# Kernel optimization log

Measured on AMD Instinct MI355X. Metric: run time of the kernel, lower is better.

Reference implementation:

```python
import jax, jax.numpy as jnp
import numpy as np

N = 8192      # number of patches (nodes)
DIN = 384     # input feature dim
DH = 512      # hidden dim
K = 6         # topk neighbors
NC = 2        # n_classes


def setup_inputs() -> dict:
    key = jax.random.key(0)
    ks = jax.random.split(key, 20)
    def w(k, shape):
        fan_in = shape[0]
        return jax.random.normal(k, shape, dtype=jnp.float32) * (1.0 / np.sqrt(fan_in))
    return {
        "x_s":   jax.random.normal(ks[0], (N, DIN), dtype=jnp.float32),
        "fc1_w": w(ks[1], (DIN, DH)), "fc1_b": jnp.zeros((DH,), jnp.float32),
        "wh_w":  w(ks[2], (DH, DH)),  "wh_b":  jnp.zeros((DH,), jnp.float32),
        "wt_w":  w(ks[3], (DH, DH)),  "wt_b":  jnp.zeros((DH,), jnp.float32),
        "l1_w":  w(ks[4], (DH, DH)),  "l1_b":  jnp.zeros((DH,), jnp.float32),
        "l2_w":  w(ks[5], (DH, DH)),  "l2_b":  jnp.zeros((DH,), jnp.float32),
        "att1_w": w(ks[6], (DH, DH // 2)), "att1_b": jnp.zeros((DH // 2,), jnp.float32),
        "att2_w": w(ks[7], (DH // 2, 1)),  "att2_b": jnp.zeros((1,), jnp.float32),
        "ln_g":  jnp.ones((DH,), jnp.float32), "ln_b": jnp.zeros((DH,), jnp.float32),
        "fc_w":  w(ks[8], (DH, NC)), "fc_b": jnp.zeros((NC,), jnp.float32),
    }


def reference(x_s, fc1_w, fc1_b, wh_w, wh_b, wt_w, wt_b,
              l1_w, l1_b, l2_w, l2_b, att1_w, att1_b, att2_w, att2_b,
              ln_g, ln_b, fc_w, fc_b):
    lrelu = jax.nn.leaky_relu  # negative_slope=0.01, torch default
    # _fc1 + mean-centering mix (batch dim of 1 dropped; mean is over nodes)
    x = lrelu(x_s @ fc1_w + fc1_b)                       # [N, DH]
    x = (x + x.mean(axis=0, keepdims=True)) * 0.5
    e_h = x @ wh_w + wh_b                                # [N, DH]
    e_t = x @ wt_w + wt_b                                # [N, DH]
    scale = DH ** -0.5
    attn_logit = (e_h * scale) @ e_t.T                   # [N, N] dense scores
    topk_w, topk_i = jax.lax.top_k(attn_logit, K)        # [N, K]
    Nb_h = e_t[topk_i]                                   # gather neighbors [N, K, DH]
    p = jax.nn.softmax(topk_w, axis=1)[..., None]        # [N, K, 1]
    eh_r = p * Nb_h + (1.0 - p) * e_h[:, None, :]        # outer-product form == broadcast
    gate = jnp.tanh(e_h[:, None, :] + eh_r)              # [N, K, DH]
    ka = jnp.einsum('nkd,nkd->nk', Nb_h, gate)           # [N, K]
    ka_p = jax.nn.softmax(ka, axis=1)
    e_Nh = jnp.einsum('nk,nkd->nd', ka_p, Nb_h)          # [N, DH]
    # bi-interaction aggregation (dropout = identity in eval)
    emb = lrelu((e_h + e_Nh) @ l1_w + l1_b) + lrelu((e_h * e_Nh) @ l2_w + l2_b)
    # global attention readout over nodes
    a = lrelu(emb @ att1_w + att1_b) @ att2_w + att2_b   # [N, 1]
    g = jax.nn.softmax(a, axis=0)
    h = (g * emb).sum(axis=0, keepdims=True)             # [1, DH]
    # layernorm (eps=1e-5)
    mu = h.mean(axis=-1, keepdims=True)
    var = ((h - mu) ** 2).mean(axis=-1, keepdims=True)
    hn = (h - mu) / jnp.sqrt(var + 1e-5) * ln_g + ln_b
    logits = hn @ fc_w + fc_b                            # [1, NC]
    return logits
```

## Files before the change

### kernel.cpp

```cpp
#include <hip/hip_runtime.h>
#include <hip/hip_bf16.h>
#include <math.h>

#define N_NODES 8192
#define DIN 384
#define DH 512
#define KNB 6
#define NEG_SLOPE 0.01f
#define NSPLIT 4

typedef __attribute__((ext_vector_type(8))) short bf16x8;
typedef __attribute__((ext_vector_type(4))) float f32x4;

__device__ __forceinline__ unsigned short f2bf(float x) {
  unsigned int u = __float_as_uint(x);
  unsigned int r = (u + 0x7fffu + ((u >> 16) & 1u)) >> 16;
  return (unsigned short)r;
}
__device__ __forceinline__ float bf2f(unsigned short u) {
  return __uint_as_float(((unsigned int)u) << 16);
}

__global__ __launch_bounds__(256) void prep_weights(
    const float* __restrict__ w0, const float* __restrict__ w1,
    const float* __restrict__ w2, const float* __restrict__ w3,
    const float* __restrict__ w4, const float* __restrict__ w5,
    unsigned short* __restrict__ pool) {
  const int f = blockIdx.x * 256 + threadIdx.x;
  const int E0 = 196608, E1 = 458752, E2 = 720896, E3 = 983040, E4 = 1245184, E5 = 1376256;
  if (f >= E5) return;
  const float* src; int off, Kw, Nw;
  if (f < E0)      { src = w0; off = 0;  Kw = 384; Nw = 512; }
  else if (f < E1) { src = w1; off = E0; Kw = 512; Nw = 512; }
  else if (f < E2) { src = w2; off = E1; Kw = 512; Nw = 512; }
  else if (f < E3) { src = w3; off = E2; Kw = 512; Nw = 512; }
  else if (f < E4) { src = w4; off = E3; Kw = 512; Nw = 512; }
  else             { src = w5; off = E4; Kw = 512; Nw = 256; }
  const int local = f - off;
  const int n = local / Kw, k = local - n * Kw;
  pool[f] = f2bf(src[(size_t)k * Nw + n]);
}

__global__ __launch_bounds__(256) void convert_xs(const float* __restrict__ xs,
                                                  unsigned short* __restrict__ out) {
  const size_t i = ((size_t)blockIdx.x * 256 + threadIdx.x) * 4;
  const float4 v = *reinterpret_cast<const float4*>(xs + i);
  ushort4 o;
  o.x = f2bf(v.x); o.y = f2bf(v.y); o.z = f2bf(v.z); o.w = f2bf(v.w);
  *reinterpret_cast<ushort4*>(out + i) = o;
}

template <int ACT, int WF32, int WBF16>
__global__ __launch_bounds__(256) void gemm128(
    const unsigned short* __restrict__ A, const unsigned short* __restrict__ Wt,
    const float* __restrict__ bias, float* __restrict__ C,
    unsigned short* __restrict__ Cb, int K, int N) {
  __shared__ unsigned short sa[128 * 64];
  __shared__ unsigned short sb[128 * 64];
  const int tid = threadIdx.x;
  const int wave = tid >> 6, lane = tid & 63;
  const int lo16 = lane & 15, hi = lane >> 4;
  const int wr = (wave >> 1) << 6, wc = (wave & 1) << 6;
  const int row0 = blockIdx.y << 7, col0 = blockIdx.x << 7;
  f32x4 acc[4][4];
#pragma unroll
  for (int rt = 0; rt < 4; ++rt)
#pragma unroll
    for (int ct = 0; ct < 4; ++ct) { acc[rt][ct].x = 0.f; acc[rt][ct].y = 0.f; acc[rt][ct].z = 0.f; acc[rt][ct].w = 0.f; }
  for (int k0 = 0; k0 < K; k0 += 64) {
    __syncthreads();
#pragma unroll
    for (int i = 0; i < 4; ++i) {
      const int c = i * 256 + tid;
      const int r = c >> 3, i8 = c & 7;
      const bf16x8 va = *reinterpret_cast<const bf16x8*>(A + (size_t)(row0 + r) * K + k0 + i8 * 8);
      const bf16x8 vb = *reinterpret_cast<const bf16x8*>(Wt + (size_t)(col0 + r) * K + k0 + i8 * 8);
      const int byte = r * 128 + ((i8 * 16) ^ ((r & 7) << 4));
      *reinterpret_cast<bf16x8*>(reinterpret_cast<char*>(sa) + byte) = va;
      *reinterpret_cast<bf16x8*>(reinterpret_cast<char*>(sb) + byte) = vb;
    }
    __syncthreads();
#pragma unroll
    for (int kk2 = 0; kk2 < 2; ++kk2) {
      const int inner = (kk2 << 6) + (hi << 4);
      bf16x8 af[4], bf[4];
#pragma unroll
      for (int t = 0; t < 4; ++t) {
        const int row = wr + t * 16 + lo16;
        af[t] = *reinterpret_cast<const bf16x8*>(reinterpret_cast<const char*>(sa) + row * 128 + (inner ^ ((row & 7) << 4)));
        const int col = wc + t * 16 + lo16;
        bf[t] = *reinterpret_cast<const bf16x8*>(reinterpret_cast<const char*>(sb) + col * 128 + (inner ^ ((col & 7) << 4)));
      }
#pragma unroll
      for (int rt = 0; rt < 4; ++rt)
#pragma unroll
        for (int ct = 0; ct < 4; ++ct)
          acc[rt][ct] = __builtin_amdgcn_mfma_f32_16x16x32_bf16(af[rt], bf[ct], acc[rt][ct], 0, 0, 0);
    }
  }
#pragma unroll
  for (int ct = 0; ct < 4; ++ct) {
    const int colg = col0 + wc + ct * 16 + lo16;
    const float bv = bias[colg];
#pragma unroll
    for (int rt = 0; rt < 4; ++rt) {
#pragma unroll
      for (int j = 0; j < 4; ++j) {
        const int r = row0 + wr + rt * 16 + hi * 4 + j;
        float v = acc[rt][ct][j] + bv;
        if (ACT) v = v > 0.f ? v : NEG_SLOPE * v;
        if (WF32) C[(size_t)r * N + colg] = v;
        if (WBF16) Cb[(size_t)r * N + colg] = f2bf(v);
      }
    }
  }
}

__global__ __launch_bounds__(256) void gemm128_ehet(
    const unsigned short* __restrict__ A,
    const unsigned short* __restrict__ W1, const unsigned short* __restrict__ W2,
    const float* __restrict__ b1, const float* __restrict__ b2,
    float* __restrict__ C1, unsigned short* __restrict__ EHb,
    float* __restrict__ C2, unsigned short* __restrict__ ETp, float kscale) {
  __shared__ unsigned short sa[128 * 64];
  __shared__ unsigned short sb1[128 * 64];
  __shared__ unsigned short sb2[128 * 64];
  const int tid = threadIdx.x;
  const int wave = tid >> 6, lane = tid & 63;
  const int lo16 = lane & 15, hi = lane >> 4;
  const int wr = (wave >> 1) << 6, wc = (wave & 1) << 6;
  const int row0 = blockIdx.y << 7, col0 = blockIdx.x << 7;
  f32x4 au[4][4], av[4][4];
#pragma unroll
  for (int rt = 0; rt < 4; ++rt)
#pragma unroll
    for (int ct = 0; ct < 4; ++ct) {
      au[rt][ct].x = 0.f; au[rt][ct].y = 0.f; au[rt][ct].z = 0.f; au[rt][ct].w = 0.f;
      av[rt][ct].x = 0.f; av[rt][ct].y = 0.f; av[rt][ct].z = 0.f; av[rt][ct].w = 0.f;
    }
  for (int k0 = 0; k0 < DH; k0 += 64) {
    __syncthreads();
#pragma unroll
    for (int i = 0; i < 4; ++i) {
      const int c = i * 256 + tid;
      const int r = c >> 3, i8 = c & 7;
      const int byte = r * 128 + ((i8 * 16) ^ ((r & 7) << 4));
      *reinterpret_cast<bf16x8*>(reinterpret_cast<char*>(sa) + byte) =
          *reinterpret_cast<const bf16x8*>(A + (size_t)(row0 + r) * DH + k0 + i8 * 8);
      *reinterpret_cast<bf16x8*>(reinterpret_cast<char*>(sb1) + byte) =
          *reinterpret_cast<const bf16x8*>(W1 + (size_t)(col0 + r) * DH + k0 + i8 * 8);
      *reinterpret_cast<bf16x8*>(reinterpret_cast<char*>(sb2) + byte) =
          *reinterpret_cast<const bf16x8*>(W2 + (size_t)(col0 + r) * DH + k0 + i8 * 8);
    }
    __syncthreads();
#pragma unroll
    for (int kk2 = 0; kk2 < 2; ++kk2) {
      const int inner = (kk2 << 6) + (hi << 4);
      bf16x8 af[4], bf1[4], bf2[4];
#pragma unroll
      for (int t = 0; t < 4; ++t) {
        const int row = wr + t * 16 + lo16;
        const int aoff = row * 128 + (inner ^ ((row & 7) << 4));
        af[t] = *reinterpret_cast<const bf16x8*>(reinterpret_cast<const char*>(sa) + aoff);
        const int col = wc + t * 16 + lo16;
        const int boff = col * 128 + (inner ^ ((col & 7) << 4));
        bf1[t] = *reinterpret_cast<const bf16x8*>(reinterpret_cast<const char*>(sb1) + boff);
        bf2[t] = *reinterpret_cast<const bf16x8*>(reinterpret_cast<const char*>(sb2) + boff);
      }
#pragma unroll
      for (int rt = 0; rt < 4; ++rt)
#pragma unroll
        for (int ct = 0; ct < 4; ++ct) {
          au[rt][ct] = __builtin_amdgcn_mfma_f32_16x16x32_bf16(af[rt], bf1[ct], au[rt][ct], 0, 0, 0);
          av[rt][ct] = __builtin_amdgcn_mfma_f32_16x16x32_bf16(af[rt], bf2[ct], av[rt][ct], 0, 0, 0);
        }
    }
  }
#pragma unroll
  for (int ct = 0; ct < 4; ++ct) {
    const int colg = col0 + wc + ct * 16 + lo16;
    const float bv1 = b1[colg], bv2 = b2[colg];
#pragma unroll
    for (int rt = 0; rt < 4; ++rt) {
#pragma unroll
      for (int j = 0; j < 4; ++j) {
        const int r = row0 + wr + rt * 16 + hi * 4 + j;
        const float vh = au[rt][ct][j] + bv1;
        const float vt = av[rt][ct][j] + bv2;
        C1[(size_t)r * DH + colg] = vh;
        EHb[(size_t)r * DH + colg] = f2bf(vh * kscale);
        C2[(size_t)r * DH + colg] = vt;
        const size_t idx = (size_t)(r >> 4) * 8192 + (size_t)(colg >> 5) * 512 +
                           (size_t)((((colg & 31) >> 3) * 16 + (r & 15)) * 8) + (colg & 7);
        ETp[idx] = f2bf(vt);
      }
    }
  }
}

__global__ __launch_bounds__(256) void gemm128_l1l2(
    const unsigned short* __restrict__ Ub, const unsigned short* __restrict__ Vb,
    const unsigned short* __restrict__ W1, const unsigned short* __restrict__ W2,
    const float* __restrict__ b1, const float* __restrict__ b2,
    unsigned short* __restrict__ EMBb) {
  __shared__ unsigned short sa1[128 * 64];
  __shared__ unsigned short sa2[128 * 64];
  __shared__ unsigned short sb1[128 * 64];
  __shared__ unsigned short sb2[128 * 64];
  const int tid = threadIdx.x;
  const int wave = tid >> 6, lane = tid & 63;
  const int lo16 = lane & 15, hi = lane >> 4;
  const int wr = (wave >> 1) << 6, wc = (wave & 1) << 6;
  const int row0 = blockIdx.y << 7, col0 = blockIdx.x << 7;
  f32x4 au[4][4], av[4][4];
#pragma unroll
  for (int rt = 0; rt < 4; ++rt)
#pragma unroll
    for (int ct = 0; ct < 4; ++ct) {
      au[rt][ct].x = 0.f; au[rt][ct].y = 0.f; au[rt][ct].z = 0.f; au[rt][ct].w = 0.f;
      av[rt][ct].x = 0.f; av[rt][ct].y = 0.f; av[rt][ct].z = 0.f; av[rt][ct].w = 0.f;
    }
  for (int k0 = 0; k0 < DH; k0 += 64) {
    __syncthreads();
#pragma unroll
    for (int i = 0; i < 4; ++i) {
      const int c = i * 256 + tid;
      const int r = c >> 3, i8 = c & 7;
      const int byte = r * 128 + ((i8 * 16) ^ ((r & 7) << 4));
      *reinterpret_cast<bf16x8*>(reinterpret_cast<char*>(sa1) + byte) =
          *reinterpret_cast<const bf16x8*>(Ub + (size_t)(row0 + r) * DH + k0 + i8 * 8);
      *reinterpret_cast<bf16x8*>(reinterpret_cast<char*>(sa2) + byte) =
          *reinterpret_cast<const bf16x8*>(Vb + (size_t)(row0 + r) * DH + k0 + i8 * 8);
      *reinterpret_cast<bf16x8*>(reinterpret_cast<char*>(sb1) + byte) =
          *reinterpret_cast<const bf16x8*>(W1 + (size_t)(col0 + r) * DH + k0 + i8 * 8);
      *reinterpret_cast<bf16x8*>(reinterpret_cast<char*>(sb2) + byte) =
          *reinterpret_cast<const bf16x8*>(W2 + (size_t)(col0 + r) * DH + k0 + i8 * 8);
    }
    __syncthreads();
#pragma unroll
    for (int kk2 = 0; kk2 < 2; ++kk2) {
      const int inner = (kk2 << 6) + (hi << 4);
      bf16x8 a1[4], a2[4], bf1[4], bf2[4];
#pragma unroll
      for (int t = 0; t < 4; ++t) {
        const int row = wr + t * 16 + lo16;
        const int aoff = row * 128 + (inner ^ ((row & 7) << 4));
        a1[t] = *reinterpret_cast<const bf16x8*>(reinterpret_cast<const char*>(sa1) + aoff);
        a2[t] = *reinterpret_cast<const bf16x8*>(reinterpret_cast<const char*>(sa2) + aoff);
        const int col = wc + t * 16 + lo16;
        const int boff = col * 128 + (inner ^ ((col & 7) << 4));
        bf1[t] = *reinterpret_cast<const bf16x8*>(reinterpret_cast<const char*>(sb1) + boff);
        bf2[t] = *reinterpret_cast<const bf16x8*>(reinterpret_cast<const char*>(sb2) + boff);
      }
#pragma unroll
      for (int rt = 0; rt < 4; ++rt)
#pragma unroll
        for (int ct = 0; ct < 4; ++ct) {
          au[rt][ct] = __builtin_amdgcn_mfma_f32_16x16x32_bf16(a1[rt], bf1[ct], au[rt][ct], 0, 0, 0);
          av[rt][ct] = __builtin_amdgcn_mfma_f32_16x16x32_bf16(a2[rt], bf2[ct], av[rt][ct], 0, 0, 0);
        }
    }
  }
#pragma unroll
  for (int ct = 0; ct < 4; ++ct) {
    const int colg = col0 + wc + ct * 16 + lo16;
    const float bv1 = b1[colg], bv2 = b2[colg];
#pragma unroll
    for (int rt = 0; rt < 4; ++rt) {
#pragma unroll
      for (int j = 0; j < 4; ++j) {
        const int r = row0 + wr + rt * 16 + hi * 4 + j;
        float u = au[rt][ct][j] + bv1;
        float v = av[rt][ct][j] + bv2;
        u = u > 0.f ? u : NEG_SLOPE * u;
        v = v > 0.f ? v : NEG_SLOPE * v;
        EMBb[(size_t)r * DH + colg] = f2bf(u + v);
      }
    }
  }
}

__global__ __launch_bounds__(256) void colsum_kernel(const float* __restrict__ X,
                                                     float* __restrict__ cs) {
  const int tid = threadIdx.x;
  float s0 = 0.f, s1 = 0.f;
  const int r0 = blockIdx.x * 128;
  for (int r = r0; r < r0 + 128; ++r) {
    s0 += X[(size_t)r * DH + tid];
    s1 += X[(size_t)r * DH + tid + 256];
  }
  atomicAdd(&cs[tid], s0);
  atomicAdd(&cs[tid + 256], s1);
}

__global__ __launch_bounds__(256) void mix_kernel(float* __restrict__ X,
                                                  const float* __restrict__ cs,
                                                  unsigned short* __restrict__ Xb) {
  const size_t gid = (size_t)blockIdx.x * 256 + threadIdx.x;
  const int c4 = ((int)gid & 127) << 2;
  float4 x = *reinterpret_cast<float4*>(X + gid * 4);
  const float inv = 1.f / 8192.f;
  x.x = (x.x + cs[c4 + 0] * inv) * 0.5f;
  x.y = (x.y + cs[c4 + 1] * inv) * 0.5f;
  x.z = (x.z + cs[c4 + 2] * inv) * 0.5f;
  x.w = (x.w + cs[c4 + 3] * inv) * 0.5f;
  ushort4 o;
  o.x = f2bf(x.x); o.y = f2bf(x.y); o.z = f2bf(x.z); o.w = f2bf(x.w);
  *reinterpret_cast<ushort4*>(Xb + gid * 4) = o;
}

__global__ __launch_bounds__(256, 4) void score_topk_v6(
    const unsigned short* __restrict__ EHb, const unsigned short* __restrict__ ETp,
    float* __restrict__ tkv, int* __restrict__ tki) {
  __shared__ unsigned short sa[32 * 512];
  __shared__ float swb[4][8 * 36];
  const int tid = threadIdx.x;
  const int wave = tid >> 6, lane = tid & 63;
  const int lo16 = lane & 15, hi = lane >> 4;
  const int bid = blockIdx.x;
  const int split = (bid & 7) >> 1;
  const int rowblk = ((bid >> 3) << 1) | (bid & 1);
  const int grow0 = rowblk << 5;
  const int colbase0 = split << 11;

#pragma unroll
  for (int i = 0; i < 8; ++i) {
    const int c = i * 256 + tid;
    const int row = c >> 6, i8 = c & 63;
    const bf16x8 v = *reinterpret_cast<const bf16x8*>(
        EHb + (size_t)(grow0 + row) * DH + i8 * 8);
    const int byte = row * 1024 + ((i8 * 16) ^ ((row & 7) << 4));
    *reinterpret_cast<bf16x8*>(reinterpret_cast<char*>(sa) + byte) = v;
  }
  __syncthreads();

  float tv[6];
  int ti[6];
#pragma unroll
  for (int s = 0; s < 6; ++s) { tv[s] = -3.4e38f; ti[s] = 0; }

  float* sw = swb[wave];
  const int scanr = lane & 31, scang = lane >> 5;

  bf16x8 bcur[4];
  {
    const int jg0 = (colbase0 + wave * 64) >> 4;
#pragma unroll
    for (int ct = 0; ct < 4; ++ct)
      bcur[ct] = *reinterpret_cast<const bf16x8*>(
          ETp + (size_t)(jg0 + ct) * 8192 + lane * 8);
  }

  for (int jt = 0; jt < 8; ++jt) {
    const int wcol0 = colbase0 + jt * 256 + wave * 64;
    const int jgbase = wcol0 >> 4;
    f32x4 acc[2][4];
#pragma unroll
    for (int rt = 0; rt < 2; ++rt)
#pragma unroll
      for (int ct = 0; ct < 4; ++ct) {
        acc[rt][ct].x = 0.f; acc[rt][ct].y = 0.f; acc[rt][ct].z = 0.f; acc[rt][ct].w = 0.f;
      }
#pragma unroll
    for (int kk = 0; kk < 16; ++kk) {
      bf16x8 bnxt[4];
      if (kk < 15) {
#pragma unroll
        for (int ct = 0; ct < 4; ++ct)
          bnxt[ct] = *reinterpret_cast<const bf16x8*>(
              ETp + (size_t)(jgbase + ct) * 8192 + (kk + 1) * 512 + lane * 8);
      } else {
        const int jtn = (jt == 7) ? 7 : (jt + 1);
        const int jgn = (colbase0 + jtn * 256 + wave * 64) >> 4;
#pragma unroll
        for (int ct = 0; ct < 4; ++ct)
          bnxt[ct] = *reinterpret_cast<const bf16x8*>(
              ETp + (size_t)(jgn + ct) * 8192 + lane * 8);
      }
      const int inner = (kk << 6) + (hi << 4);
#pragma unroll
      for (int rt = 0; rt < 2; ++rt) {
        const int row = rt * 16 + lo16;
        const bf16x8 af = *reinterpret_cast<const bf16x8*>(
            reinterpret_cast<const char*>(sa) + row * 1024 + (inner ^ ((row & 7) << 4)));
#pragma unroll
        for (int ct = 0; ct < 4; ++ct)
          acc[rt][ct] = __builtin_amdgcn_mfma_f32_16x16x32_bf16(af, bcur[ct], acc[rt][ct], 0, 0, 0);
      }
#pragma unroll
      for (int ct = 0; ct < 4; ++ct) bcur[ct] = bnxt[ct];
    }
#pragma unroll
    for (int ct = 0; ct < 4; ++ct) {
#pragma unroll
      for (int h = 0; h < 2; ++h) {
        if ((lo16 >> 3) == h) {
#pragma unroll
          for (int rt = 0; rt < 2; ++rt)
            *reinterpret_cast<f32x4*>(sw + (lo16 & 7) * 36 + rt * 16 + hi * 4) = acc[rt][ct];
        }
        asm volatile("s_waitcnt lgkmcnt(0)" ::: "memory");
#pragma unroll
        for (int cc = 0; cc < 4; ++cc) {
          const float v = sw[(scang * 4 + cc) * 36 + scanr];
          const int col = wcol0 + ct * 16 + h * 8 + scang * 4 + cc;
          if (v > tv[5]) {
            tv[5] = v; ti[5] = col;
#pragma unroll
            for (int p = 5; p > 0; --p) {
              if (tv[p] > tv[p - 1]) {
                float tvt = tv[p]; tv[p] = tv[p - 1]; tv[p - 1] = tvt;
                int tit = ti[p]; ti[p] = ti[p - 1]; ti[p - 1] = tit;
              }
            }
          }
        }
        asm volatile("s_waitcnt lgkmcnt(0)" ::: "memory");
      }
    }
  }
  __syncthreads();
  float* mv = reinterpret_cast<float*>(sa);
  int* mi = reinterpret_cast<int*>(mv + 32 * 8 * 6);
  {
    const int li = wave * 2 + scang;
#pragma unroll
    for (int s = 0; s < 6; ++s) {
      mv[(scanr * 8 + li) * 6 + s] = tv[s];
      mi[(scanr * 8 + li) * 6 + s] = ti[s];
    }
  }
  __syncthreads();
  if (tid < 32) {
    int pq[8] = {0, 0, 0, 0, 0, 0, 0, 0};
    const int base = (split * N_NODES + grow0 + tid) * 6;
    for (int s = 0; s < 6; ++s) {
      float best = -3.4e38f;
      int bi = 0x7fffffff, bq = 0;
#pragma unroll
      for (int q = 0; q < 8; ++q) {
        if (pq[q] < 6) {
          const float v = mv[(tid * 8 + q) * 6 + pq[q]];
          const int ix = mi[(tid * 8 + q) * 6 + pq[q]];
          if (v > best || (v == best && ix < bi)) { best = v; bi = ix; bq = q; }
        }
      }
      tkv[base + s] = best;
      tki[base + s] = bi;
#pragma unroll
      for (int q = 0; q < 8; ++q) pq[q] += (bq == q) ? 1 : 0;
    }
  }
}

__global__ __launch_bounds__(256) void merge_topk4(const float* __restrict__ tkv,
                                                   const int* __restrict__ tki,
                                                   float* __restrict__ fw,
                                                   int* __restrict__ fi) {
  const int n = blockIdx.x * 256 + threadIdx.x;
  int pq[NSPLIT] = {0, 0, 0, 0};
  for (int s = 0; s < 6; ++s) {
    float best = -3.4e38f;
    int bi = 0x7fffffff, bq = 0;
#pragma unroll
    for (int q = 0; q < NSPLIT; ++q) {
      if (pq[q] < 6) {
        const float v = tkv[((size_t)q * N_NODES + n) * 6 + pq[q]];
        const int ix = tki[((size_t)q * N_NODES + n) * 6 + pq[q]];
        if (v > best || (v == best && ix < bi)) { best = v; bi = ix; bq = q; }
      }
    }
    fw[n * 6 + s] = best;
    fi[n * 6 + s] = bi;
#pragma unroll
    for (int q = 0; q < NSPLIT; ++q) pq[q] += (bq == q) ? 1 : 0;
  }
}

__global__ __launch_bounds__(256) void agg_kernel(const float* __restrict__ EH,
                                                  const float* __restrict__ ET,
                                                  const float* __restrict__ fw,
                                                  const int* __restrict__ fi,
                                                  unsigned short* __restrict__ Ub,
                                                  unsigned short* __restrict__ Vb) {
  __shared__ float sNb[KNB][DH];
  __shared__ float sred[4][8];
  __shared__ float ska[8];
  const int node = blockIdx.x;
  const int tid = threadIdx.x;
  float w[KNB];
  int idx[KNB];
#pragma unroll
  for (int k = 0; k < KNB; ++k) {
    w[k] = fw[node * KNB + k];
    idx[k] = fi[node * KNB + k];
  }
  float mx = w[0];
#pragma unroll
  for (int k = 1; k < KNB; ++k) mx = fmaxf(mx, w[k]);
  float pk[KNB];
  float se = 0.f;
#pragma unroll
  for (int k = 0; k < KNB; ++k) { pk[k] = expf(w[k] - mx); se += pk[k]; }
  const float inv_se = 1.f / se;
#pragma unroll
  for (int k = 0; k < KNB; ++k) pk[k] *= inv_se;
  for (int e = tid; e < KNB * DH; e += 256) {
    int k = e >> 9, d = e & 511;
    sNb[k][d] = ET[(size_t)idx[k] * DH + d];
  }
  __syncthreads();
  float eh[2];
  eh[0] = EH[(size_t)node * DH + tid];
  eh[1] = EH[(size_t)node * DH + tid + 256];
  float ka[KNB] = {0, 0, 0, 0, 0, 0};
#pragma unroll
  for (int t = 0; t < 2; ++t) {
    const int d = tid + t * 256;
    const float e_ = eh[t];
#pragma unroll
    for (int k = 0; k < KNB; ++k) {
      float Nb = sNb[k][d];
      float ehr = pk[k] * Nb + (1.f - pk[k]) * e_;
      float g = tanhf(e_ + ehr);
      ka[k] = fmaf(Nb, g, ka[k]);
    }
  }
#pragma unroll
  for (int k = 0; k < KNB; ++k) {
    float v = ka[k];
#pragma unroll
    for (int off = 32; off > 0; off >>= 1) v += __shfl_down(v, off, 64);
    if ((tid & 63) == 0) sred[tid >> 6][k] = v;
  }
  __syncthreads();
  if (tid < KNB) ska[tid] = sred[0][tid] + sred[1][tid] + sred[2][tid] + sred[3][tid];
  __syncthreads();
  float kav[KNB];
#pragma unroll
  for (int k = 0; k < KNB; ++k) kav[k] = ska[k];
  float kmx = kav[0];
#pragma unroll
  for (int k = 1; k < KNB; ++k) kmx = fmaxf(kmx, kav[k]);
  float kp[KNB];
  float ks = 0.f;
#pragma unroll
  for (int k = 0; k < KNB; ++k) { kp[k] = expf(kav[k] - kmx); ks += kp[k]; }
  const float inv_ks = 1.f / ks;
#pragma unroll
  for (int k = 0; k < KNB; ++k) kp[k] *= inv_ks;
#pragma unroll
  for (int t = 0; t < 2; ++t) {
    const int d = tid + t * 256;
    float eNh = 0.f;
#pragma unroll
    for (int k = 0; k < KNB; ++k) eNh = fmaf(kp[k], sNb[k][d], eNh);
    const float e_ = eh[t];
    Ub[(size_t)node * DH + d] = f2bf(e_ + eNh);
    Vb[(size_t)node * DH + d] = f2bf(e_ * eNh);
  }
}

__global__ __launch_bounds__(256) void att_dot(const unsigned short* __restrict__ HIDb,
                                               const float* __restrict__ w2,
                                               const float* __restrict__ b2,
                                               float* __restrict__ a) {
  const int wid = threadIdx.x >> 6, lane = threadIdx.x & 63;
  const int node = blockIdx.x * 4 + wid;
  const ushort4 h4 = *reinterpret_cast<const ushort4*>(HIDb + (size_t)node * 256 + lane * 4);
  const float4 w4 = *reinterpret_cast<const float4*>(w2 + lane * 4);
  float s = bf2f(h4.x) * w4.x + bf2f(h4.y) * w4.y + bf2f(h4.z) * w4.z + bf2f(h4.w) * w4.w;
#pragma unroll
  for (int off = 32; off > 0; off >>= 1) s += __shfl_down(s, off, 64);
  if (lane == 0) a[node] = s + b2[0];
}

__global__ __launch_bounds__(1024) void softmax_stats(const float* __restrict__ a,
                                                      float* __restrict__ st) {
  __shared__ float red[16];
  __shared__ float bc;
  const int tid = threadIdx.x;
  float mx = -3.4e38f;
  for (int i = tid; i < N_NODES; i += 1024) mx = fmaxf(mx, a[i]);
#pragma unroll
  for (int off = 32; off > 0; off >>= 1) mx = fmaxf(mx, __shfl_xor(mx, off, 64));
  if ((tid & 63) == 0) red[tid >> 6] = mx;
  __syncthreads();
  if (tid == 0) {
    float m = red[0];
    for (int i = 1; i < 16; ++i) m = fmaxf(m, red[i]);
    bc = m;
  }
  __syncthreads();
  const float gm = bc;
  float se = 0.f;
  for (int i = tid; i < N_NODES; i += 1024) se += expf(a[i] - gm);
#pragma unroll
  for (int off = 32; off > 0; off >>= 1) se += __shfl_xor(se, off, 64);
  if ((tid & 63) == 0) red[tid >> 6] = se;
  __syncthreads();
  if (tid == 0) {
    float s = 0.f;
    for (int i = 0; i < 16; ++i) s += red[i];
    st[0] = gm;
    st[1] = s;
  }
}

__global__ __launch_bounds__(256) void readout(const unsigned short* __restrict__ EMBb,
                                               const float* __restrict__ a,
                                               const float* __restrict__ st,
                                               float* __restrict__ h) {
  __shared__ float sacc[4][64];
  const int tid = threadIdx.x;
  const int c = (blockIdx.x << 6) + (tid & 63);
  const int rsub = tid >> 6;
  const float mx = st[0], inv_se = 1.f / st[1];
  const int r0 = blockIdx.y << 8;
  float acc = 0.f;
  for (int i = 0; i < 64; ++i) {
    const int r = r0 + (i << 2) + rsub;
    const float g = expf(a[r] - mx);
    acc = fmaf(g, bf2f(EMBb[(size_t)r * DH + c]), acc);
  }
  sacc[rsub][tid & 63] = acc * inv_se;
  __syncthreads();
  if (rsub == 0) {
    float t = sacc[0][tid] + sacc[1][tid] + sacc[2][tid] + sacc[3][tid];
    atomicAdd(&h[c], t);
  }
}

__global__ __launch_bounds__(512) void finalize(const float* __restrict__ h,
                                                const float* __restrict__ ln_g,
                                                const float* __restrict__ ln_b,
                                                const float* __restrict__ fc_w,
                                                const float* __restrict__ fc_b,
                                                float* __restrict__ out) {
  __shared__ float red0[8];
  __shared__ float red1[8];
  __shared__ float bc[2];
  const int tid = threadIdx.x;
  const int wid = tid >> 6, lane = tid & 63;
  const float v = h[tid];
  float s = v;
#pragma unroll
  for (int off = 32; off > 0; off >>= 1) s += __shfl_xor(s, off, 64);
  if (lane == 0) red0[wid] = s;
  __syncthreads();
  if (tid == 0) {
    float t = 0.f;
    for (int i = 0; i < 8; ++i) t += red0[i];
    bc[0] = t * (1.f / 512.f);
  }
  __syncthreads();
  const float mu = bc[0];
  const float dv = v - mu;
  s = dv * dv;
#pragma unroll
  for (int off = 32; off > 0; off >>= 1) s += __shfl_xor(s, off, 64);
  if (lane == 0) red0[wid] = s;
  __syncthreads();
  if (tid == 0) {
    float t = 0.f;
    for (int i = 0; i < 8; ++i) t += red0[i];
    bc[1] = t * (1.f / 512.f);
  }
  __syncthreads();
  const float var = bc[1];
  const float hn = dv / sqrtf(var + 1e-5f) * ln_g[tid] + ln_b[tid];
  float l0 = hn * fc_w[tid * 2 + 0];
  float l1 = hn * fc_w[tid * 2 + 1];
#pragma unroll
  for (int off = 32; off > 0; off >>= 1) {
    l0 += __shfl_xor(l0, off, 64);
    l1 += __shfl_xor(l1, off, 64);
  }
  if (lane == 0) { red0[wid] = l0; red1[wid] = l1; }
  __syncthreads();
  if (tid == 0) {
    float t0 = 0.f, t1 = 0.f;
    for (int i = 0; i < 8; ++i) { t0 += red0[i]; t1 += red1[i]; }
    out[0] = t0 + fc_b[0];
    out[1] = t1 + fc_b[1];
  }
}

extern "C" void kernel_launch(void* const* d_in, const int* in_sizes, int n_in,
                              void* d_out, int out_size, void* d_ws, size_t ws_size,
                              hipStream_t stream) {
  const float* x_s    = (const float*)d_in[0];
  const float* fc1_w  = (const float*)d_in[1];
  const float* fc1_b  = (const float*)d_in[2];
  const float* wh_w   = (const float*)d_in[3];
  const float* wh_b   = (const float*)d_in[4];
  const float* wt_w   = (const float*)d_in[5];
  const float* wt_b   = (const float*)d_in[6];
  const float* l1_w   = (const float*)d_in[7];
  const float* l1_b   = (const float*)d_in[8];
  const float* l2_w   = (const float*)d_in[9];
  const float* l2_b   = (const float*)d_in[10];
  const float* att1_w = (const float*)d_in[11];
  const float* att1_b = (const float*)d_in[12];
  const float* att2_w = (const float*)d_in[13];
  const float* att2_b = (const float*)d_in[14];
  const float* ln_g   = (const float*)d_in[15];
  const float* ln_b   = (const float*)d_in[16];
  const float* fc_w   = (const float*)d_in[17];
  const float* fc_b   = (const float*)d_in[18];

  float* ws = (float*)d_ws;
  const size_t BIG = (size_t)N_NODES * DH;
  float* B1 = ws;
  float* B2 = ws + BIG;
  unsigned short* R1 = (unsigned short*)(ws + 2 * BIG);
  unsigned short* R2 = R1 + BIG;
  unsigned short* R3 = R2 + BIG;
  unsigned short* WT = R3 + BIG;
  float* tail = (float*)(WT + 1376256);
  float* tkv    = tail;
  int*   tki    = (int*)(tkv + NSPLIT * N_NODES * 6);
  float* fwv    = (float*)(tki + NSPLIT * N_NODES * 6);
  int*   fiv    = (int*)(fwv + N_NODES * 6);
  float* colsum = (float*)(fiv + N_NODES * 6);
  float* av     = colsum + DH;
  float* stats  = av + N_NODES;
  float* hbuf   = stats + 16;

  unsigned short* fc1t  = WT + 0;
  unsigned short* wht   = WT + 196608;
  unsigned short* wtt   = WT + 458752;
  unsigned short* l1t   = WT + 720896;
  unsigned short* l2t   = WT + 983040;
  unsigned short* att1t = WT + 1245184;

  const float kscale = 0.044194173824159216f;

  prep_weights<<<5376, 256, 0, stream>>>(fc1_w, wh_w, wt_w, l1_w, l2_w, att1_w, WT);
  convert_xs<<<3072, 256, 0, stream>>>(x_s, R1);
  gemm128<1, 1, 0><<<dim3(4, 64), 256, 0, stream>>>(
      R1, fc1t, fc1_b, B1, nullptr, DIN, DH);
  hipMemsetAsync(colsum, 0, DH * sizeof(float), stream);
  colsum_kernel<<<64, 256, 0, stream>>>(B1, colsum);
  mix_kernel<<<4096, 256, 0, stream>>>(B1, colsum, R2);
  gemm128_ehet<<<dim3(4, 64), 256, 0, stream>>>(
      R2, wht, wtt, wh_b, wt_b, B1, R1, B2, R3, kscale);
  score_topk_v6<<<1024, 256, 0, stream>>>(R1, R3, tkv, tki);
  merge_topk4<<<32, 256, 0, stream>>>(tkv, tki, fwv, fiv);
  agg_kernel<<<N_NODES, 256, 0, stream>>>(B1, B2, fwv, fiv, R1, R2);
  gemm128_l1l2<<<dim3(4, 64), 256, 0, stream>>>(
      R1, R2, l1t, l2t, l1_b, l2_b, R3);
  gemm128<1, 0, 1><<<dim3(2, 64), 256, 0, stream>>>(
      R3, att1t, att1_b, nullptr, R1, DH, 256);
  att_dot<<<2048, 256, 0, stream>>>(R1, att2_w, att2_b, av);
  softmax_stats<<<1, 1024, 0, stream>>>(av, stats);
  hipMemsetAsync(hbuf, 0, DH * sizeof(float), stream);
  readout<<<dim3(8, 32), 256, 0, stream>>>(R3, av, stats, hbuf);
  finalize<<<1, 512, 0, stream>>>(hbuf, ln_g, ln_b, fc_w, fc_b, (float*)d_out);
}
```

Before: 357.1 us.

## Tile weight transpose, widen GEMM blocks to 512 threads, store EH/ET as bf16

Several changes at once. The weight prep now transposes through a 64x64 shared-memory tile so both reads and writes are coalesced, instead of a strided per-element gather. All GEMM kernels move to 512 threads (8 waves, 32-column wave tiles), which halves the accumulators per thread and raises occupancy. The e_h/e_t GEMM drops its fp32 outputs and writes bf16 copies instead, with the attention scale moved into merge_topk. The aggregation kernel then reads bf16 neighbours with vector loads, cutting global traffic at some precision cost.

```diff
diff --git a/kernel.cpp b/kernel.cpp
--- a/kernel.cpp
+++ b/kernel.cpp
@@ -8,6 +8,7 @@
 #define KNB 6
 #define NEG_SLOPE 0.01f
 #define NSPLIT 4
+#define KSCALE 0.044194173824159216f
 
 typedef __attribute__((ext_vector_type(8))) short bf16x8;
 typedef __attribute__((ext_vector_type(4))) float f32x4;
@@ -21,24 +22,34 @@
   return __uint_as_float(((unsigned int)u) << 16);
 }
 
-__global__ __launch_bounds__(256) void prep_weights(
+__global__ __launch_bounds__(256) void prep_weights_t(
     const float* __restrict__ w0, const float* __restrict__ w1,
     const float* __restrict__ w2, const float* __restrict__ w3,
     const float* __restrict__ w4, const float* __restrict__ w5,
     unsigned short* __restrict__ pool) {
-  const int f = blockIdx.x * 256 + threadIdx.x;
-  const int E0 = 196608, E1 = 458752, E2 = 720896, E3 = 983040, E4 = 1245184, E5 = 1376256;
-  if (f >= E5) return;
-  const float* src; int off, Kw, Nw;
-  if (f < E0)      { src = w0; off = 0;  Kw = 384; Nw = 512; }
-  else if (f < E1) { src = w1; off = E0; Kw = 512; Nw = 512; }
-  else if (f < E2) { src = w2; off = E1; Kw = 512; Nw = 512; }
-  else if (f < E3) { src = w3; off = E2; Kw = 512; Nw = 512; }
-  else if (f < E4) { src = w4; off = E3; Kw = 512; Nw = 512; }
-  else             { src = w5; off = E4; Kw = 512; Nw = 256; }
-  const int local = f - off;
-  const int n = local / Kw, k = local - n * Kw;
-  pool[f] = f2bf(src[(size_t)k * Nw + n]);
+  __shared__ float tile[64][65];
+  const int t = blockIdx.x;
+  const float* src; int off, Kw, Nw, tl;
+  if (t < 48)       { src = w0; off = 0;       Kw = 384; Nw = 512; tl = t; }
+  else if (t < 112) { src = w1; off = 196608;  Kw = 512; Nw = 512; tl = t - 48; }
+  else if (t < 176) { src = w2; off = 458752;  Kw = 512; Nw = 512; tl = t - 112; }
+  else if (t < 240) { src = w3; off = 720896;  Kw = 512; Nw = 512; tl = t - 176; }
+  else if (t < 304) { src = w4; off = 983040;  Kw = 512; Nw = 512; tl = t - 240; }
+  else              { src = w5; off = 1245184; Kw = 512; Nw = 256; tl = t - 304; }
+  const int nk = Kw >> 6;
+  const int kbase = (tl % nk) << 6, nbase = (tl / nk) << 6;
+  const int tx = threadIdx.x & 63, ty = threadIdx.x >> 6;
+#pragma unroll
+  for (int i = 0; i < 16; ++i) {
+    const int r = i * 4 + ty;
+    tile[r][tx] = src[(size_t)(kbase + r) * Nw + nbase + tx];
+  }
+  __syncthreads();
+#pragma unroll
+  for (int i = 0; i < 16; ++i) {
+    const int rr = i * 4 + ty;
+    pool[(size_t)off + (size_t)(nbase + rr) * Kw + kbase + tx] = f2bf(tile[tx][rr]);
+  }
 }
 
 __global__ __launch_bounds__(256) void convert_xs(const float* __restrict__ xs,
@@ -51,7 +62,7 @@
 }
 
 template <int ACT, int WF32, int WBF16>
-__global__ __launch_bounds__(256) void gemm128(
+__global__ __launch_bounds__(512) void gemm128(
     const unsigned short* __restrict__ A, const unsigned short* __restrict__ Wt,
     const float* __restrict__ bias, float* __restrict__ C,
     unsigned short* __restrict__ Cb, int K, int N) {
@@ -60,46 +71,49 @@
   const int tid = threadIdx.x;
   const int wave = tid >> 6, lane = tid & 63;
   const int lo16 = lane & 15, hi = lane >> 4;
-  const int wr = (wave >> 1) << 6, wc = (wave & 1) << 6;
+  const int wr = (wave >> 2) << 6, wc = (wave & 3) << 5;
   const int row0 = blockIdx.y << 7, col0 = blockIdx.x << 7;
-  f32x4 acc[4][4];
+  f32x4 acc[4][2];
 #pragma unroll
   for (int rt = 0; rt < 4; ++rt)
 #pragma unroll
-    for (int ct = 0; ct < 4; ++ct) { acc[rt][ct].x = 0.f; acc[rt][ct].y = 0.f; acc[rt][ct].z = 0.f; acc[rt][ct].w = 0.f; }
+    for (int ct = 0; ct < 2; ++ct) { acc[rt][ct].x = 0.f; acc[rt][ct].y = 0.f; acc[rt][ct].z = 0.f; acc[rt][ct].w = 0.f; }
   for (int k0 = 0; k0 < K; k0 += 64) {
     __syncthreads();
 #pragma unroll
-    for (int i = 0; i < 4; ++i) {
-      const int c = i * 256 + tid;
+    for (int i = 0; i < 2; ++i) {
+      const int c = i * 512 + tid;
       const int r = c >> 3, i8 = c & 7;
-      const bf16x8 va = *reinterpret_cast<const bf16x8*>(A + (size_t)(row0 + r) * K + k0 + i8 * 8);
-      const bf16x8 vb = *reinterpret_cast<const bf16x8*>(Wt + (size_t)(col0 + r) * K + k0 + i8 * 8);
       const int byte = r * 128 + ((i8 * 16) ^ ((r & 7) << 4));
-      *reinterpret_cast<bf16x8*>(reinterpret_cast<char*>(sa) + byte) = va;
-      *reinterpret_cast<bf16x8*>(reinterpret_cast<char*>(sb) + byte) = vb;
+      *reinterpret_cast<bf16x8*>(reinterpret_cast<char*>(sa) + byte) =
+          *reinterpret_cast<const bf16x8*>(A + (size_t)(row0 + r) * K + k0 + i8 * 8);
+      *reinterpret_cast<bf16x8*>(reinterpret_cast<char*>(sb) + byte) =
+          *reinterpret_cast<const bf16x8*>(Wt + (size_t)(col0 + r) * K + k0 + i8 * 8);
     }
     __syncthreads();
 #pragma unroll
     for (int kk2 = 0; kk2 < 2; ++kk2) {
       const int inner = (kk2 << 6) + (hi << 4);
-      bf16x8 af[4], bf[4];
+      bf16x8 af[4], bf[2];
 #pragma unroll
       for (int t = 0; t < 4; ++t) {
         const int row = wr + t * 16 + lo16;
         af[t] = *reinterpret_cast<const bf16x8*>(reinterpret_cast<const char*>(sa) + row * 128 + (inner ^ ((row & 7) << 4)));
+      }
+#pragma unroll
+      for (int t = 0; t < 2; ++t) {
         const int col = wc + t * 16 + lo16;
         bf[t] = *reinterpret_cast<const bf16x8*>(reinterpret_cast<const char*>(sb) + col * 128 + (inner ^ ((col & 7) << 4)));
       }
 #pragma unroll
       for (int rt = 0; rt < 4; ++rt)
 #pragma unroll
-        for (int ct = 0; ct < 4; ++ct)
+        for (int ct = 0; ct < 2; ++ct)
           acc[rt][ct] = __builtin_amdgcn_mfma_f32_16x16x32_bf16(af[rt], bf[ct], acc[rt][ct], 0, 0, 0);
     }
   }
 #pragma unroll
-  for (int ct = 0; ct < 4; ++ct) {
+  for (int ct = 0; ct < 2; ++ct) {
     const int colg = col0 + wc + ct * 16 + lo16;
     const float bv = bias[colg];
 #pragma unroll
@@ -116,33 +130,33 @@
   }
 }
 
-__global__ __launch_bounds__(256) void gemm128_ehet(
+__global__ __launch_bounds__(512) void gemm128_ehet(
     const unsigned short* __restrict__ A,
     const unsigned short* __restrict__ W1, const unsigned short* __restrict__ W2,
     const float* __restrict__ b1, const float* __restrict__ b2,
-    float* __restrict__ C1, unsigned short* __restrict__ EHb,
-    float* __restrict__ C2, unsigned short* __restrict__ ETp, float kscale) {
+    unsigned short* __restrict__ EHb, unsigned short* __restrict__ ETp,
+    unsigned short* __restrict__ ETb) {
   __shared__ unsigned short sa[128 * 64];
   __shared__ unsigned short sb1[128 * 64];
   __shared__ unsigned short sb2[128 * 64];
   const int tid = threadIdx.x;
   const int wave = tid >> 6, lane = tid & 63;
   const int lo16 = lane & 15, hi = lane >> 4;
-  const int wr = (wave >> 1) << 6, wc = (wave & 1) << 6;
+  const int wr = (wave >> 2) << 6, wc = (wave & 3) << 5;
   const int row0 = blockIdx.y << 7, col0 = blockIdx.x << 7;
-  f32x4 au[4][4], av[4][4];
+  f32x4 au[4][2], av[4][2];
 #pragma unroll
   for (int rt = 0; rt < 4; ++rt)
 #pragma unroll
-    for (int ct = 0; ct < 4; ++ct) {
+    for (int ct = 0; ct < 2; ++ct) {
       au[rt][ct].x = 0.f; au[rt][ct].y = 0.f; au[rt][ct].z = 0.f; au[rt][ct].w = 0.f;
       av[rt][ct].x = 0.f; av[rt][ct].y = 0.f; av[rt][ct].z = 0.f; av[rt][ct].w = 0.f;
     }
   for (int k0 = 0; k0 < DH; k0 += 64) {
     __syncthreads();
 #pragma unroll
-    for (int i = 0; i < 4; ++i) {
-      const int c = i * 256 + tid;
+    for (int i = 0; i < 2; ++i) {
+      const int c = i * 512 + tid;
       const int r = c >> 3, i8 = c & 7;
       const int byte = r * 128 + ((i8 * 16) ^ ((r & 7) << 4));
       *reinterpret_cast<bf16x8*>(reinterpret_cast<char*>(sa) + byte) =
@@ -156,12 +170,14 @@
 #pragma unroll
     for (int kk2 = 0; kk2 < 2; ++kk2) {
       const int inner = (kk2 << 6) + (hi << 4);
-      bf16x8 af[4], bf1[4], bf2[4];
+      bf16x8 af[4], bf1[2], bf2[2];
 #pragma unroll
       for (int t = 0; t < 4; ++t) {
         const int row = wr + t * 16 + lo16;
-        const int aoff = row * 128 + (inner ^ ((row & 7) << 4));
-        af[t] = *reinterpret_cast<const bf16x8*>(reinterpret_cast<const char*>(sa) + aoff);
+        af[t] = *reinterpret_cast<const bf16x8*>(reinterpret_cast<const char*>(sa) + row * 128 + (inner ^ ((row & 7) << 4)));
+      }
+#pragma unroll
+      for (int t = 0; t < 2; ++t) {
         const int col = wc + t * 16 + lo16;
         const int boff = col * 128 + (inner ^ ((col & 7) << 4));
         bf1[t] = *reinterpret_cast<const bf16x8*>(reinterpret_cast<const char*>(sb1) + boff);
@@ -170,14 +186,14 @@
 #pragma unroll
       for (int rt = 0; rt < 4; ++rt)
 #pragma unroll
-        for (int ct = 0; ct < 4; ++ct) {
+        for (int ct = 0; ct < 2; ++ct) {
           au[rt][ct] = __builtin_amdgcn_mfma_f32_16x16x32_bf16(af[rt], bf1[ct], au[rt][ct], 0, 0, 0);
           av[rt][ct] = __builtin_amdgcn_mfma_f32_16x16x32_bf16(af[rt], bf2[ct], av[rt][ct], 0, 0, 0);
         }
     }
   }
 #pragma unroll
-  for (int ct = 0; ct < 4; ++ct) {
+  for (int ct = 0; ct < 2; ++ct) {
     const int colg = col0 + wc + ct * 16 + lo16;
     const float bv1 = b1[colg], bv2 = b2[colg];
 #pragma unroll
@@ -187,9 +203,8 @@
         const int r = row0 + wr + rt * 16 + hi * 4 + j;
         const float vh = au[rt][ct][j] + bv1;
         const float vt = av[rt][ct][j] + bv2;
-        C1[(size_t)r * DH + colg] = vh;
-        EHb[(size_t)r * DH + colg] = f2bf(vh * kscale);
-        C2[(size_t)r * DH + colg] = vt;
+        EHb[(size_t)r * DH + colg] = f2bf(vh);
+        ETb[(size_t)r * DH + colg] = f2bf(vt);
         const size_t idx = (size_t)(r >> 4) * 8192 + (size_t)(colg >> 5) * 512 +
                            (size_t)((((colg & 31) >> 3) * 16 + (r & 15)) * 8) + (colg & 7);
         ETp[idx] = f2bf(vt);
@@ -198,7 +213,7 @@
   }
 }
 
-__global__ __launch_bounds__(256) void gemm128_l1l2(
+__global__ __launch_bounds__(512) void gemm128_l1l2(
     const unsigned short* __restrict__ Ub, const unsigned short* __restrict__ Vb,
     const unsigned short* __restrict__ W1, const unsigned short* __restrict__ W2,
     const float* __restrict__ b1, const float* __restrict__ b2,
@@ -210,21 +225,21 @@
   const int tid = threadIdx.x;
   const int wave = tid >> 6, lane = tid & 63;
   const int lo16 = lane & 15, hi = lane >> 4;
-  const int wr = (wave >> 1) << 6, wc = (wave & 1) << 6;
+  const int wr = (wave >> 2) << 6, wc = (wave & 3) << 5;
   const int row0 = blockIdx.y << 7, col0 = blockIdx.x << 7;
-  f32x4 au[4][4], av[4][4];
+  f32x4 au[4][2], av[4][2];
 #pragma unroll
   for (int rt = 0; rt < 4; ++rt)
 #pragma unroll
-    for (int ct = 0; ct < 4; ++ct) {
+    for (int ct = 0; ct < 2; ++ct) {
       au[rt][ct].x = 0.f; au[rt][ct].y = 0.f; au[rt][ct].z = 0.f; au[rt][ct].w = 0.f;
       av[rt][ct].x = 0.f; av[rt][ct].y = 0.f; av[rt][ct].z = 0.f; av[rt][ct].w = 0.f;
     }
   for (int k0 = 0; k0 < DH; k0 += 64) {
     __syncthreads();
 #pragma unroll
-    for (int i = 0; i < 4; ++i) {
-      const int c = i * 256 + tid;
+    for (int i = 0; i < 2; ++i) {
+      const int c = i * 512 + tid;
       const int r = c >> 3, i8 = c & 7;
       const int byte = r * 128 + ((i8 * 16) ^ ((r & 7) << 4));
       *reinterpret_cast<bf16x8*>(reinterpret_cast<char*>(sa1) + byte) =
@@ -240,13 +255,16 @@
 #pragma unroll
     for (int kk2 = 0; kk2 < 2; ++kk2) {
       const int inner = (kk2 << 6) + (hi << 4);
-      bf16x8 a1[4], a2[4], bf1[4], bf2[4];
+      bf16x8 a1[4], a2[4], bf1[2], bf2[2];
 #pragma unroll
       for (int t = 0; t < 4; ++t) {
         const int row = wr + t * 16 + lo16;
         const int aoff = row * 128 + (inner ^ ((row & 7) << 4));
         a1[t] = *reinterpret_cast<const bf16x8*>(reinterpret_cast<const char*>(sa1) + aoff);
         a2[t] = *reinterpret_cast<const bf16x8*>(reinterpret_cast<const char*>(sa2) + aoff);
+      }
+#pragma unroll
+      for (int t = 0; t < 2; ++t) {
         const int col = wc + t * 16 + lo16;
         const int boff = col * 128 + (inner ^ ((col & 7) << 4));
         bf1[t] = *reinterpret_cast<const bf16x8*>(reinterpret_cast<const char*>(sb1) + boff);
@@ -255,14 +273,14 @@
 #pragma unroll
       for (int rt = 0; rt < 4; ++rt)
 #pragma unroll
-        for (int ct = 0; ct < 4; ++ct) {
+        for (int ct = 0; ct < 2; ++ct) {
           au[rt][ct] = __builtin_amdgcn_mfma_f32_16x16x32_bf16(a1[rt], bf1[ct], au[rt][ct], 0, 0, 0);
           av[rt][ct] = __builtin_amdgcn_mfma_f32_16x16x32_bf16(a2[rt], bf2[ct], av[rt][ct], 0, 0, 0);
         }
     }
   }
 #pragma unroll
-  for (int ct = 0; ct < 4; ++ct) {
+  for (int ct = 0; ct < 2; ++ct) {
     const int colg = col0 + wc + ct * 16 + lo16;
     const float bv1 = b1[colg], bv2 = b2[colg];
 #pragma unroll
@@ -470,15 +488,15 @@
         if (v > best || (v == best && ix < bi)) { best = v; bi = ix; bq = q; }
       }
     }
-    fw[n * 6 + s] = best;
+    fw[n * 6 + s] = best * KSCALE;
     fi[n * 6 + s] = bi;
 #pragma unroll
     for (int q = 0; q < NSPLIT; ++q) pq[q] += (bq == q) ? 1 : 0;
   }
 }
 
-__global__ __launch_bounds__(256) void agg_kernel(const float* __restrict__ EH,
-                                                  const float* __restrict__ ET,
+__global__ __launch_bounds__(256) void agg_kernel(const unsigned short* __restrict__ EHb,
+                                                  const unsigned short* __restrict__ ETb,
                                                   const float* __restrict__ fw,
                                                   const int* __restrict__ fi,
                                                   unsigned short* __restrict__ Ub,
@@ -505,14 +523,16 @@
   const float inv_se = 1.f / se;
 #pragma unroll
   for (int k = 0; k < KNB; ++k) pk[k] *= inv_se;
-  for (int e = tid; e < KNB * DH; e += 256) {
-    int k = e >> 9, d = e & 511;
-    sNb[k][d] = ET[(size_t)idx[k] * DH + d];
+#pragma unroll
+  for (int k = 0; k < KNB; ++k) {
+    const ushort2 v = *reinterpret_cast<const ushort2*>(ETb + (size_t)idx[k] * DH + tid * 2);
+    sNb[k][tid * 2] = bf2f(v.x);
+    sNb[k][tid * 2 + 1] = bf2f(v.y);
   }
   __syncthreads();
   float eh[2];
-  eh[0] = EH[(size_t)node * DH + tid];
-  eh[1] = EH[(size_t)node * DH + tid + 256];
+  eh[0] = bf2f(EHb[(size_t)node * DH + tid]);
+  eh[1] = bf2f(EHb[(size_t)node * DH + tid + 256]);
   float ka[KNB] = {0, 0, 0, 0, 0, 0};
 #pragma unroll
   for (int t = 0; t < 2; ++t) {
@@ -712,11 +732,11 @@
   float* ws = (float*)d_ws;
   const size_t BIG = (size_t)N_NODES * DH;
   float* B1 = ws;
-  float* B2 = ws + BIG;
-  unsigned short* R1 = (unsigned short*)(ws + 2 * BIG);
+  unsigned short* R1 = (unsigned short*)(ws + BIG);
   unsigned short* R2 = R1 + BIG;
   unsigned short* R3 = R2 + BIG;
-  unsigned short* WT = R3 + BIG;
+  unsigned short* R4 = R3 + BIG;
+  unsigned short* WT = R4 + BIG;
   float* tail = (float*)(WT + 1376256);
   float* tkv    = tail;
   int*   tki    = (int*)(tkv + NSPLIT * N_NODES * 6);
@@ -734,27 +754,25 @@
   unsigned short* l2t   = WT + 983040;
   unsigned short* att1t = WT + 1245184;
 
-  const float kscale = 0.044194173824159216f;
-
-  prep_weights<<<5376, 256, 0, stream>>>(fc1_w, wh_w, wt_w, l1_w, l2_w, att1_w, WT);
+  prep_weights_t<<<336, 256, 0, stream>>>(fc1_w, wh_w, wt_w, l1_w, l2_w, att1_w, WT);
   convert_xs<<<3072, 256, 0, stream>>>(x_s, R1);
-  gemm128<1, 1, 0><<<dim3(4, 64), 256, 0, stream>>>(
+  gemm128<1, 1, 0><<<dim3(4, 64), 512, 0, stream>>>(
       R1, fc1t, fc1_b, B1, nullptr, DIN, DH);
   hipMemsetAsync(colsum, 0, DH * sizeof(float), stream);
   colsum_kernel<<<64, 256, 0, stream>>>(B1, colsum);
   mix_kernel<<<4096, 256, 0, stream>>>(B1, colsum, R2);
-  gemm128_ehet<<<dim3(4, 64), 256, 0, stream>>>(
-      R2, wht, wtt, wh_b, wt_b, B1, R1, B2, R3, kscale);
+  gemm128_ehet<<<dim3(4, 64), 512, 0, stream>>>(
+      R2, wht, wtt, wh_b, wt_b, R1, R3, R4);
   score_topk_v6<<<1024, 256, 0, stream>>>(R1, R3, tkv, tki);
   merge_topk4<<<32, 256, 0, stream>>>(tkv, tki, fwv, fiv);
-  agg_kernel<<<N_NODES, 256, 0, stream>>>(B1, B2, fwv, fiv, R1, R2);
-  gemm128_l1l2<<<dim3(4, 64), 256, 0, stream>>>(
-      R1, R2, l1t, l2t, l1_b, l2_b, R3);
-  gemm128<1, 0, 1><<<dim3(2, 64), 256, 0, stream>>>(
-      R3, att1t, att1_b, nullptr, R1, DH, 256);
-  att_dot<<<2048, 256, 0, stream>>>(R1, att2_w, att2_b, av);
+  agg_kernel<<<N_NODES, 256, 0, stream>>>(R1, R4, fwv, fiv, R2, R3);
+  gemm128_l1l2<<<dim3(4, 64), 512, 0, stream>>>(
+      R2, R3, l1t, l2t, l1_b, l2_b, R1);
+  gemm128<1, 0, 1><<<dim3(2, 64), 512, 0, stream>>>(
+      R1, att1t, att1_b, nullptr, R2, DH, 256);
+  att_dot<<<2048, 256, 0, stream>>>(R2, att2_w, att2_b, av);
   softmax_stats<<<1, 1024, 0, stream>>>(av, stats);
   hipMemsetAsync(hbuf, 0, DH * sizeof(float), stream);
-  readout<<<dim3(8, 32), 256, 0, stream>>>(R3, av, stats, hbuf);
+  readout<<<dim3(8, 32), 256, 0, stream>>>(R1, av, stats, hbuf);
   finalize<<<1, 512, 0, stream>>>(hbuf, ln_g, ln_b, fc_w, fc_b, (float*)d_out);
 }
```

Measured after the change: 336.4 us. 1.06x faster.
